# Kernel optimization log

Measured on AMD Instinct MI355X. Metric: run time of the kernel, lower is better.

## Reference

```python
import jax, jax.numpy as jnp
import numpy as np
from jax import lax

B, E, H, L, P, IMG, NCLS = 8, 768, 12, 12, 16, 224, 1000
D = E // H
MLP = 4 * E
SCALE = D ** -0.5
NPATCH = (IMG // P) ** 2  # 196
N = NPATCH + 1             # 197 with cls token
INIT_VAL = 0.1


def _ln(x, g, b, eps=1e-5):
    mu = jnp.mean(x, -1, keepdims=True)
    var = jnp.mean((x - mu) ** 2, -1, keepdims=True)
    return (x - mu) / jnp.sqrt(var + eps) * g + b


def _wasserstein(q, cov_q, k, cov_k):
    # 2-Wasserstein distance matrix between diagonal Gaussians (STOSA style)
    mean_term = (-2.0 * jnp.einsum('bhnd,bhmd->bhnm', q, k)
                 + jnp.sum(q * q, -1)[..., :, None]
                 + jnp.sum(k * k, -1)[..., None, :])
    sq_q = jnp.sqrt(jnp.clip(cov_q, 1e-24))
    sq_k = jnp.sqrt(jnp.clip(cov_k, 1e-24))
    cov_term = (-2.0 * jnp.einsum('bhnd,bhmd->bhnm', sq_q, sq_k)
                + jnp.sum(cov_q, -1)[..., :, None]
                + jnp.sum(cov_k, -1)[..., None, :])
    return mean_term + cov_term


def _patch_embed(x, w, b):
    # x: [B,3,IMG,IMG], w: [E,3,P,P] -> [B, NPATCH, E]
    y = lax.conv_general_dilated(x, w, (P, P), 'VALID',
                                 dimension_numbers=('NCHW', 'OIHW', 'NCHW'))
    y = y + b[None, :, None, None]
    return y.reshape(x.shape[0], E, -1).transpose(0, 2, 1)


def _mlp(x, w1, b1, w2, b2):
    return jax.nn.gelu(x @ w1.T + b1, approximate=False) @ w2.T + b2


def setup_inputs() -> dict:
    key = jax.random.key(0)
    ks = jax.random.split(key, 32)
    s = 0.02
    inp = {
        'x': jax.random.normal(ks[0], (B, 3, IMG, IMG), jnp.float32),
        'rel_pos_bias': jax.random.normal(ks[1], (H, N, N), jnp.float32),
        'patch_w': jax.random.normal(ks[2], (E, 3, P, P), jnp.float32) * s,
        'patch_b': jnp.zeros((E,), jnp.float32),
        'cov_patch_w': jax.random.normal(ks[3], (E, 3, P, P), jnp.float32) * s,
        'cov_patch_b': jnp.zeros((E,), jnp.float32),
        'cls_tok': jax.random.normal(ks[4], (1, 1, E), jnp.float32) * s,
        'cov_cls_tok': jax.random.normal(ks[5], (1, 1, E), jnp.float32) * s,
        'norm1_g': jnp.ones((L, E), jnp.float32),
        'norm1_b': jnp.zeros((L, E), jnp.float32),
        'qkv_w': jax.random.normal(ks[6], (L, 3 * E, E), jnp.float32) * s,
        'q_bias': jnp.zeros((L, E), jnp.float32),
        'v_bias': jnp.zeros((L, E), jnp.float32),
        'cov_q_bias': jnp.zeros((L, E), jnp.float32),
        'cov_v_bias': jnp.zeros((L, E), jnp.float32),
        'proj_w': jax.random.normal(ks[7], (L, E, E), jnp.float32) * s,
        'proj_b': jnp.zeros((L, E), jnp.float32),
        'cov_proj_w': jax.random.normal(ks[8], (L, E, E), jnp.float32) * s,
        'cov_proj_b': jnp.zeros((L, E), jnp.float32),
        'gamma1': jnp.full((L, E), INIT_VAL, jnp.float32),
        'gamma2': jnp.full((L, E), INIT_VAL, jnp.float32),
        'norm2_g': jnp.ones((L, E), jnp.float32),
        'norm2_b': jnp.zeros((L, E), jnp.float32),
        'fc1_w': jax.random.normal(ks[9], (L, MLP, E), jnp.float32) * s,
        'fc1_b': jnp.zeros((L, MLP), jnp.float32),
        'fc2_w': jax.random.normal(ks[10], (L, E, MLP), jnp.float32) * s,
        'fc2_b': jnp.zeros((L, E), jnp.float32),
        'fc_norm_g': jnp.ones((E,), jnp.float32),
        'fc_norm_b': jnp.zeros((E,), jnp.float32),
        'head_w': jax.random.normal(ks[11], (NCLS, E), jnp.float32) * s,
        'head_b': jnp.zeros((NCLS,), jnp.float32),
    }
    # fix_init_weight rescaling: proj / cov_proj / fc2 divided by sqrt(2*layer_id)
    resc = 1.0 / jnp.sqrt(2.0 * jnp.arange(1, L + 1, dtype=jnp.float32))
    inp['proj_w'] = inp['proj_w'] * resc[:, None, None]
    inp['cov_proj_w'] = inp['cov_proj_w'] * resc[:, None, None]
    inp['fc2_w'] = inp['fc2_w'] * resc[:, None, None]
    return inp


def reference(x, rel_pos_bias, patch_w, patch_b, cov_patch_w, cov_patch_b,
              cls_tok, cov_cls_tok, norm1_g, norm1_b, qkv_w, q_bias, v_bias,
              cov_q_bias, cov_v_bias, proj_w, proj_b, cov_proj_w, cov_proj_b,
              gamma1, gamma2, norm2_g, norm2_b, fc1_w, fc1_b, fc2_w, fc2_b,
              fc_norm_g, fc_norm_b, head_w, head_b):
    b = x.shape[0]
    xm = _patch_embed(x, patch_w, patch_b)
    xc = _patch_embed(x, cov_patch_w, cov_patch_b)
    xm = jnp.concatenate([jnp.broadcast_to(cls_tok, (b, 1, E)), xm], 1)
    xc = jnp.concatenate([jnp.broadcast_to(cov_cls_tok, (b, 1, E)), xc], 1)
    n = xm.shape[1]

    for i in range(L):
        xm_n = _ln(xm, norm1_g[i], norm1_b[i])
        xc_n = _ln(xc, norm1_g[i], norm1_b[i])  # shared norm1, as in source
        qkvb = jnp.concatenate([q_bias[i], jnp.zeros_like(v_bias[i]), v_bias[i]])
        cov_qkvb = jnp.concatenate([cov_q_bias[i], jnp.zeros_like(cov_v_bias[i]), cov_v_bias[i]])
        qkv = (xm_n @ qkv_w[i].T + qkvb).reshape(b, n, 3, H, D).transpose(2, 0, 3, 1, 4)
        q, k, v = qkv[0], qkv[1], qkv[2]
        # NOTE: source (bug-faithfully) uses qkv.weight for the cov path too
        cqkv = jax.nn.elu(xc_n @ qkv_w[i].T + cov_qkvb) + 1.0
        cqkv = cqkv.reshape(b, n, 3, H, D).transpose(2, 0, 3, 1, 4)
        cq, ck, cv = cqkv[0], cqkv[1], cqkv[2]
        q = q * SCALE
        attn = jax.nn.sigmoid(-_wasserstein(q, cq, k, ck) + 1e-24)
        attn = jax.nn.softmax(attn + rel_pos_bias, axis=-1)  # [B,H,N,N]
        mean_ctx = jnp.einsum('bhnm,bhmd->bhnd', attn, v).transpose(0, 2, 1, 3).reshape(b, n, E)
        cov_ctx = jnp.einsum('bhnm,bhmd->bhnd', attn * attn, cv).transpose(0, 2, 1, 3).reshape(b, n, E)
        mh = mean_ctx @ proj_w[i].T + proj_b[i]
        ch = cov_ctx @ cov_proj_w[i].T + cov_proj_b[i]
        xm = xm + gamma1[i] * mh
        xm = xm + gamma2[i] * _mlp(_ln(xm, norm2_g[i], norm2_b[i]), fc1_w[i], fc1_b[i], fc2_w[i], fc2_b[i])
        xc = xc + gamma1[i] * ch
        xc = xc + gamma2[i] * _mlp(_ln(xc, norm2_g[i], norm2_b[i]), fc1_w[i], fc1_b[i], fc2_w[i], fc2_b[i])

    t = jnp.mean(xm[:, 1:], axis=1)          # mean pooling over patch tokens
    t = _ln(t, fc_norm_g, fc_norm_b)
    return t @ head_w.T + head_b              # [B, num_classes]
```

## Files before the change

### kernel.cpp

```cpp
#include <hip/hip_runtime.h>
#include <hip/hip_bf16.h>
#include <math.h>

#define BB 8
#define EE 768
#define HH 12
#define LL 12
#define DD 64
#define MLPD 3072
#define NN 197
#define NPATCH 196
#define NCLS 1000
#define NROWS (BB*NN)
#define PROWS (BB*NPATCH)
#define MPAD 1664
#define HTILES 13
#define NBH (BB*HH)
#define NP224 224
#define NP256 256
#define SCALE 0.125f

#define MODE_F32   0
#define MODE_ELU1F 1
#define MODE_GELUB 2
#define MODE_RESF  3

typedef __attribute__((ext_vector_type(8))) short bf16x8;
typedef __attribute__((ext_vector_type(4))) float f32x4;

__device__ __forceinline__ unsigned short f2b(float f) {
    union { __hip_bfloat16 h; unsigned short u; } x;
    x.h = __float2bfloat16(f);
    return x.u;
}

#define GLD(gptr, lptr) __builtin_amdgcn_global_load_lds( \
    (const __attribute__((address_space(1))) unsigned int*)(gptr), \
    (__attribute__((address_space(3))) unsigned int*)(lptr), 16, 0, 0)

__global__ __launch_bounds__(256) void mfma_gemm2(
    const unsigned short* __restrict__ A0, const unsigned short* __restrict__ A1,
    const unsigned short* __restrict__ W0, const unsigned short* __restrict__ W1,
    const float* __restrict__ bias0, const float* __restrict__ bias1,
    int K, int Nc, int mode0, int mode1,
    const float* __restrict__ gamma,
    const float* __restrict__ resid0, const float* __restrict__ resid1,
    float* __restrict__ Cf0, float* __restrict__ Cf1,
    unsigned short* __restrict__ Cb0, unsigned short* __restrict__ Cb1)
{
    __shared__ unsigned short lA[128 * 32];
    __shared__ unsigned short lB[128 * 32];
    const int tid  = threadIdx.x;
    const int lane = tid & 63;
    const int wave = tid >> 6;
    const int wm = wave >> 1, wn = wave & 1;
    const int half = blockIdx.y >= HTILES;
    const int mout0 = (blockIdx.y - (half ? HTILES : 0)) * 128;
    const int n0 = blockIdx.x * 128;
    const unsigned short* A = half ? A1 : A0;
    const unsigned short* W = half ? W1 : W0;
    const float* bias = half ? bias1 : bias0;
    const float* resid = half ? resid1 : resid0;
    float* Cf = half ? Cf1 : Cf0;
    unsigned short* Cb = half ? Cb1 : Cb0;
    const int mode = half ? mode1 : mode0;

    const int srow  = lane >> 2;
    const int skoff = (lane & 3) * 8;
    const int fr = lane & 15;
    const int fk = (lane >> 4) * 8;

    f32x4 acc[4][4];
#pragma unroll
    for (int i = 0; i < 4; i++)
#pragma unroll
        for (int j = 0; j < 4; j++) acc[i][j] = (f32x4){0.f, 0.f, 0.f, 0.f};

    for (int k0 = 0; k0 < K; k0 += 32) {
#pragma unroll
        for (int i = 0; i < 2; i++) {
            int chunk = wave * 2 + i;
            int row = chunk * 16 + srow;
            GLD(A + (size_t)(mout0 + row) * K + k0 + skoff, lA + chunk * 512);
            GLD(W + (size_t)(n0 + row) * K + k0 + skoff, lB + chunk * 512);
        }
        __syncthreads();
        bf16x8 a[4], b[4];
#pragma unroll
        for (int t = 0; t < 4; t++) {
            a[t] = *(const bf16x8*)(lA + (wm * 64 + t * 16 + fr) * 32 + fk);
            b[t] = *(const bf16x8*)(lB + (wn * 64 + t * 16 + fr) * 32 + fk);
        }
#pragma unroll
        for (int i = 0; i < 4; i++)
#pragma unroll
            for (int j = 0; j < 4; j++)
                acc[i][j] = __builtin_amdgcn_mfma_f32_16x16x32_bf16(a[i], b[j], acc[i][j], 0, 0, 0);
        __syncthreads();
    }

    const int crow0 = mout0 + wm * 64;
    const int ccol0 = n0 + wn * 64;
    const int lr = (lane >> 4) * 4;
    const int lc = lane & 15;
#pragma unroll
    for (int i = 0; i < 4; i++) {
#pragma unroll
        for (int j = 0; j < 4; j++) {
            int col = ccol0 + j * 16 + lc;
            float bv = bias ? bias[col] : 0.f;
#pragma unroll
            for (int r = 0; r < 4; r++) {
                int row = crow0 + i * 16 + lr + r;
                float v = acc[i][j][r] + bv;
                size_t o = (size_t)row * Nc + col;
                if (mode == MODE_ELU1F) {
                    Cf[o] = (v > 0.f) ? (v + 1.f) : expf(v);
                } else if (mode == MODE_GELUB) {
                    v = 0.5f * v * (1.f + erff(v * 0.70710678118654752f));
                    Cb[o] = f2b(v);
                } else if (mode == MODE_RESF) {
                    Cf[o] = resid[o] + gamma[col] * v;
                } else {
                    Cf[o] = v;
                }
            }
        }
    }
}

__global__ __launch_bounds__(256) void mfma_gemm2_sk(
    const unsigned short* __restrict__ A0, const unsigned short* __restrict__ A1,
    const unsigned short* __restrict__ W0, const unsigned short* __restrict__ W1,
    int K, int Kc, int Nc, int S,
    float* __restrict__ P)
{
    __shared__ unsigned short lA[128 * 32];
    __shared__ unsigned short lB[128 * 32];
    const int tid  = threadIdx.x;
    const int lane = tid & 63;
    const int wave = tid >> 6;
    const int wm = wave >> 1, wn = wave & 1;
    const int half = blockIdx.y >= HTILES;
    const int mout0 = (blockIdx.y - (half ? HTILES : 0)) * 128;
    const int n0 = blockIdx.x * 128;
    const int z = blockIdx.z;
    const int kb = z * Kc;
    const unsigned short* A = half ? A1 : A0;
    const unsigned short* W = half ? W1 : W0;

    const int srow  = lane >> 2;
    const int skoff = (lane & 3) * 8;
    const int fr = lane & 15;
    const int fk = (lane >> 4) * 8;

    f32x4 acc[4][4];
#pragma unroll
    for (int i = 0; i < 4; i++)
#pragma unroll
        for (int j = 0; j < 4; j++) acc[i][j] = (f32x4){0.f, 0.f, 0.f, 0.f};

    for (int k0 = kb; k0 < kb + Kc; k0 += 32) {
#pragma unroll
        for (int i = 0; i < 2; i++) {
            int chunk = wave * 2 + i;
            int row = chunk * 16 + srow;
            GLD(A + (size_t)(mout0 + row) * K + k0 + skoff, lA + chunk * 512);
            GLD(W + (size_t)(n0 + row) * K + k0 + skoff, lB + chunk * 512);
        }
        __syncthreads();
        bf16x8 a[4], b[4];
#pragma unroll
        for (int t = 0; t < 4; t++) {
            a[t] = *(const bf16x8*)(lA + (wm * 64 + t * 16 + fr) * 32 + fk);
            b[t] = *(const bf16x8*)(lB + (wn * 64 + t * 16 + fr) * 32 + fk);
        }
#pragma unroll
        for (int i = 0; i < 4; i++)
#pragma unroll
            for (int j = 0; j < 4; j++)
                acc[i][j] = __builtin_amdgcn_mfma_f32_16x16x32_bf16(a[i], b[j], acc[i][j], 0, 0, 0);
        __syncthreads();
    }

    float* Pout = P + (size_t)(half * S + z) * MPAD * Nc;
    const int crow0 = mout0 + wm * 64;
    const int ccol0 = n0 + wn * 64;
    const int lr = (lane >> 4) * 4;
    const int lc = lane & 15;
#pragma unroll
    for (int i = 0; i < 4; i++) {
#pragma unroll
        for (int j = 0; j < 4; j++) {
            int col = ccol0 + j * 16 + lc;
#pragma unroll
            for (int r = 0; r < 4; r++) {
                int row = crow0 + i * 16 + lr + r;
                Pout[(size_t)row * Nc + col] = acc[i][j][r];
            }
        }
    }
}

__global__ __launch_bounds__(256) void sk_reduce_kernel(
    const float* __restrict__ P, int S, int Nc, int mode,
    const float* __restrict__ bias0, const float* __restrict__ bias1,
    const float* __restrict__ gamma,
    const float* __restrict__ resid0, const float* __restrict__ resid1,
    float* __restrict__ C0, float* __restrict__ C1)
{
    const size_t per = (size_t)MPAD * Nc;
    size_t gi = ((size_t)blockIdx.x * 256 + threadIdx.x) * 4;
    if (gi >= per) return;
    const int half = blockIdx.y;
    const float* p = P + (size_t)half * S * per + gi;
    float4 s = *(const float4*)p;
    for (int z = 1; z < S; z++) {
        float4 q = *(const float4*)(p + (size_t)z * per);
        s.x += q.x; s.y += q.y; s.z += q.z; s.w += q.w;
    }
    const int col = (int)(gi % (size_t)Nc);
    const float* bias = half ? bias1 : bias0;
    float4 bv = *(const float4*)(bias + col);
    s.x += bv.x; s.y += bv.y; s.z += bv.z; s.w += bv.w;
    float* C = half ? C1 : C0;
    if (mode == MODE_RESF) {
        const float* resid = half ? resid1 : resid0;
        float4 rv = *(const float4*)(resid + gi);
        float4 gv = *(const float4*)(gamma + col);
        s.x = rv.x + gv.x * s.x;
        s.y = rv.y + gv.y * s.y;
        s.z = rv.z + gv.z * s.z;
        s.w = rv.w + gv.w * s.w;
    }
    *(float4*)(C + gi) = s;
}

__global__ __launch_bounds__(256) void pre_kernel(
    const float* __restrict__ qkv, const float* __restrict__ cqkv,
    unsigned short* __restrict__ Aq, unsigned short* __restrict__ Bk,
    float* __restrict__ rsum, float* __restrict__ csum,
    unsigned short* __restrict__ vT, unsigned short* __restrict__ cvT)
{
    const int t = blockIdx.x;
    const int bh = blockIdx.y;
    const int b = bh / HH, h = bh % HH;
    const int n0 = t * 64;
    const int lane = threadIdx.x & 63;
    const int w = threadIdx.x >> 6;
    __shared__ unsigned short vs[64][66];
    __shared__ unsigned short cvs[64][66];

    for (int p = 0; p < 16; p++) {
        int nl = p * 4 + w;
        int n = n0 + nl;
        int d = lane;
        size_t arow = ((size_t)bh * NP256 + n) * 128;
        if (n < NN) {
            size_t basei = (size_t)(b * NN + n) * 3 * EE + h * DD + d;
            float q  = qkv[basei];
            float k  = qkv[basei + EE];
            float v  = qkv[basei + 2 * EE];
            float cq = cqkv[basei];
            float ck = cqkv[basei + EE];
            float cv = cqkv[basei + 2 * EE];
            float qs = q * SCALE;
            float sqq = sqrtf(fmaxf(cq, 1e-24f));
            float sqk = sqrtf(fmaxf(ck, 1e-24f));
            Aq[arow + d]      = f2b(qs);
            Aq[arow + 64 + d] = f2b(sqq);
            Bk[arow + d]      = f2b(k);
            Bk[arow + 64 + d] = f2b(sqk);
            vs[nl][d]  = f2b(v);
            cvs[nl][d] = f2b(cv);
            float r = qs * qs + cq;
            float c = k * k + ck;
            for (int off2 = 32; off2 > 0; off2 >>= 1) {
                r += __shfl_down(r, off2);
                c += __shfl_down(c, off2);
            }
            if (d == 0) { rsum[bh * NP256 + n] = r; csum[bh * NP256 + n] = c; }
        } else {
            ((unsigned int*)(Aq + arow))[d] = 0u;
            ((unsigned int*)(Bk + arow))[d] = 0u;
            vs[nl][d] = 0; cvs[nl][d] = 0;
            if (d == 0) { rsum[bh * NP256 + n] = 0.f; csum[bh * NP256 + n] = 0.f; }
        }
    }
    __syncthreads();
    for (int p = 0; p < 16; p++) {
        int dr = p * 4 + w;
        int n = n0 + lane;
        if (n < NP224) {
            vT [((size_t)bh * 64 + dr) * NP224 + n] = vs[lane][dr];
            cvT[((size_t)bh * 64 + dr) * NP224 + n] = cvs[lane][dr];
        }
    }
}

__global__ __launch_bounds__(256) void wass_gemm(
    const unsigned short* __restrict__ Aq, const unsigned short* __restrict__ Bk,
    const float* __restrict__ rsum, const float* __restrict__ csum,
    const float* __restrict__ rpb, float* __restrict__ S)
{
    __shared__ unsigned short lA[128 * 32];
    __shared__ unsigned short lB[128 * 32];
    const int tid = threadIdx.x, lane = tid & 63, wave = tid >> 6;
    const int wm = wave >> 1, wn = wave & 1;
    const int bh = blockIdx.z;
    const int h = bh % HH;
    const int m0 = blockIdx.y * 128;
    const int n0 = blockIdx.x * 128;
    const unsigned short* A = Aq + (size_t)bh * NP256 * 128;
    const unsigned short* B = Bk + (size_t)bh * NP256 * 128;
    const int srow = lane >> 2, skoff = (lane & 3) * 8;
    const int fr = lane & 15, fk = (lane >> 4) * 8;

    f32x4 acc[4][4];
#pragma unroll
    for (int i = 0; i < 4; i++)
#pragma unroll
        for (int j = 0; j < 4; j++) acc[i][j] = (f32x4){0.f, 0.f, 0.f, 0.f};

    for (int k0 = 0; k0 < 128; k0 += 32) {
#pragma unroll
        for (int i = 0; i < 2; i++) {
            int chunk = wave * 2 + i;
            int row = chunk * 16 + srow;
            GLD(A + (size_t)(m0 + row) * 128 + k0 + skoff, lA + chunk * 512);
            GLD(B + (size_t)(n0 + row) * 128 + k0 + skoff, lB + chunk * 512);
        }
        __syncthreads();
        bf16x8 a[4], b[4];
#pragma unroll
        for (int t = 0; t < 4; t++) {
            a[t] = *(const bf16x8*)(lA + (wm * 64 + t * 16 + fr) * 32 + fk);
            b[t] = *(const bf16x8*)(lB + (wn * 64 + t * 16 + fr) * 32 + fk);
        }
#pragma unroll
        for (int i = 0; i < 4; i++)
#pragma unroll
            for (int j = 0; j < 4; j++)
                acc[i][j] = __builtin_amdgcn_mfma_f32_16x16x32_bf16(a[i], b[j], acc[i][j], 0, 0, 0);
        __syncthreads();
    }

    const int lr = (lane >> 4) * 4;
    const int lc = lane & 15;
#pragma unroll
    for (int i = 0; i < 4; i++) {
#pragma unroll
        for (int j = 0; j < 4; j++) {
            int m = n0 + wn * 64 + j * 16 + lc;
            float cs = csum[bh * NP256 + m];
#pragma unroll
            for (int r = 0; r < 4; r++) {
                int n = m0 + wm * 64 + i * 16 + lr + r;
                float z = 2.f * acc[i][j][r] - rsum[bh * NP256 + n] - cs + 1e-24f;
                float s = 1.f / (1.f + expf(-z));
                float rp = (n < NN && m < NN) ? rpb[((size_t)h * NN + n) * NN + m] : 0.f;
                S[((size_t)bh * NP256 + n) * NP256 + m] = s + rp;
            }
        }
    }
}

__global__ __launch_bounds__(256) void softmax_kernel(
    const float* __restrict__ S, unsigned short* __restrict__ Ab,
    unsigned short* __restrict__ A2b)
{
    const int wave = threadIdx.x >> 6, lane = threadIdx.x & 63;
    const int idx = blockIdx.x * 4 + wave;
    if (idx >= NBH * NN) return;
    const int bh = idx / NN, n = idx % NN;
    const float* row = S + ((size_t)bh * NP256 + n) * NP256;
    float l[4], mx = -1e30f;
#pragma unroll
    for (int j = 0; j < 4; j++) {
        int m = lane + j * 64;
        l[j] = (m < NN) ? row[m] : -1e30f;
        mx = fmaxf(mx, l[j]);
    }
    for (int off = 32; off > 0; off >>= 1) mx = fmaxf(mx, __shfl_xor(mx, off));
    float e[4], sum = 0.f;
#pragma unroll
    for (int j = 0; j < 4; j++) {
        int m = lane + j * 64;
        e[j] = (m < NN) ? expf(l[j] - mx) : 0.f;
        sum += e[j];
    }
    for (int off = 32; off > 0; off >>= 1) sum += __shfl_xor(sum, off);
    float inv = 1.f / sum;
    unsigned short* ar  = Ab  + ((size_t)bh * NP256 + n) * NP224;
    unsigned short* ar2 = A2b + ((size_t)bh * NP256 + n) * NP224;
#pragma unroll
    for (int j = 0; j < 4; j++) {
        int m = lane + j * 64;
        if (m < NP224) {
            float p = e[j] * inv;
            ar[m]  = f2b(p);
            ar2[m] = f2b(p * p);
        }
    }
}

__global__ __launch_bounds__(256) void ctx_gemm(
    const unsigned short* __restrict__ Ab, const unsigned short* __restrict__ A2b,
    const unsigned short* __restrict__ vT, const unsigned short* __restrict__ cvT,
    unsigned short* __restrict__ ctxm, unsigned short* __restrict__ ctxc)
{
    __shared__ unsigned short lA1[128 * 32];
    __shared__ unsigned short lA2[128 * 32];
    __shared__ unsigned short lB[128 * 32];
    const int tid = threadIdx.x, lane = tid & 63, wave = tid >> 6;
    const int wm = wave >> 1, wn = wave & 1;
    const int bh = blockIdx.y;
    const int b = bh / HH, h = bh % HH;
    const int m0 = blockIdx.x * 128;
    const int srow = lane >> 2, skoff = (lane & 3) * 8;
    const int fr = lane & 15, fk = (lane >> 4) * 8;

    f32x4 acc[4][4];
#pragma unroll
    for (int i = 0; i < 4; i++)
#pragma unroll
        for (int j = 0; j < 4; j++) acc[i][j] = (f32x4){0.f, 0.f, 0.f, 0.f};

    for (int k0 = 0; k0 < NP224; k0 += 32) {
#pragma unroll
        for (int i = 0; i < 2; i++) {
            int chunk = wave * 2 + i;
            int row = chunk * 16 + srow;
            size_t aoff = ((size_t)bh * NP256 + m0 + row) * NP224 + k0 + skoff;
            GLD(Ab + aoff,  lA1 + chunk * 512);
            GLD(A2b + aoff, lA2 + chunk * 512);
            const unsigned short* bsrc = (chunk < 4)
                ? (vT  + ((size_t)bh * 64 + row) * NP224)
                : (cvT + ((size_t)bh * 64 + row - 64) * NP224);
            GLD(bsrc + k0 + skoff, lB + chunk * 512);
        }
        __syncthreads();
        const unsigned short* asrc = wn ? lA2 : lA1;
        bf16x8 a[4], bfr[4];
#pragma unroll
        for (int t = 0; t < 4; t++) {
            a[t]   = *(const bf16x8*)(asrc + (wm * 64 + t * 16 + fr) * 32 + fk);
            bfr[t] = *(const bf16x8*)(lB   + (wn * 64 + t * 16 + fr) * 32 + fk);
        }
#pragma unroll
        for (int i = 0; i < 4; i++)
#pragma unroll
            for (int j = 0; j < 4; j++)
                acc[i][j] = __builtin_amdgcn_mfma_f32_16x16x32_bf16(a[i], bfr[j], acc[i][j], 0, 0, 0);
        __syncthreads();
    }

    const int lr = (lane >> 4) * 4;
    const int lc = lane & 15;
    unsigned short* dst = wn ? ctxc : ctxm;
#pragma unroll
    for (int i = 0; i < 4; i++) {
#pragma unroll
        for (int j = 0; j < 4; j++) {
            int dcol = j * 16 + lc;
#pragma unroll
            for (int r = 0; r < 4; r++) {
                int n = m0 + wm * 64 + i * 16 + lr + r;
                if (n >= NN) continue;
                dst[((size_t)(b * NN + n)) * EE + h * DD + dcol] = f2b(acc[i][j][r]);
            }
        }
    }
}

__global__ __launch_bounds__(256) void gemm_kernel(
    const float* __restrict__ A, const float* __restrict__ W,
    const float* __restrict__ bias, float* __restrict__ C,
    int M, int Nc, int K)
{
    __shared__ float As[16][64];
    __shared__ float Bs[16][64];
    const int tid = threadIdx.x;
    const int tm = tid >> 4;
    const int tn = tid & 15;
    const int m0 = blockIdx.y * 64;
    const int n0 = blockIdx.x * 64;
    float acc[4][4] = {};
    for (int k0 = 0; k0 < K; k0 += 16) {
#pragma unroll
        for (int i = 0; i < 4; i++) {
            int idx = tid + i * 256;
            int r = idx >> 4;
            int c = idx & 15;
            int gm = m0 + r;
            As[c][r] = (gm < M) ? A[(size_t)gm * K + k0 + c] : 0.f;
            int gn = n0 + r;
            Bs[c][r] = (gn < Nc) ? W[(size_t)gn * K + k0 + c] : 0.f;
        }
        __syncthreads();
#pragma unroll
        for (int kk = 0; kk < 16; kk++) {
            float a[4], b[4];
#pragma unroll
            for (int i = 0; i < 4; i++) a[i] = As[kk][tm * 4 + i];
#pragma unroll
            for (int j = 0; j < 4; j++) b[j] = Bs[kk][tn * 4 + j];
#pragma unroll
            for (int i = 0; i < 4; i++)
#pragma unroll
                for (int j = 0; j < 4; j++)
                    acc[i][j] += a[i] * b[j];
        }
        __syncthreads();
    }
#pragma unroll
    for (int i = 0; i < 4; i++) {
        int gm = m0 + tm * 4 + i;
        if (gm >= M) continue;
#pragma unroll
        for (int j = 0; j < 4; j++) {
            int gn = n0 + tn * 4 + j;
            if (gn >= Nc) continue;
            C[(size_t)gm * Nc + gn] = acc[i][j] + (bias ? bias[gn] : 0.f);
        }
    }
}

__global__ __launch_bounds__(256) void cvt_kernel(
    const float* __restrict__ src, unsigned short* __restrict__ dst, int n)
{
    int i = (blockIdx.x * 256 + threadIdx.x) * 4;
    if (i >= n) return;
    float4 f = *(const float4*)(src + i);
    ushort4 u;
    u.x = f2b(f.x); u.y = f2b(f.y); u.z = f2b(f.z); u.w = f2b(f.w);
    *(ushort4*)(dst + i) = u;
}

#define W_QKV   0
#define W_PROJ  1769472
#define W_CPROJ 2359296
#define W_FC1   2949120
#define W_FC2   5308416
#define W_TOTAL 7667712

__global__ __launch_bounds__(256) void cvt_layer_kernel(
    const float* __restrict__ qkvw, const float* __restrict__ pw,
    const float* __restrict__ cpw, const float* __restrict__ f1,
    const float* __restrict__ f2, unsigned short* __restrict__ dst)
{
    int i = (blockIdx.x * 256 + threadIdx.x) * 4;
    if (i >= W_TOTAL) return;
    const float* s; int off;
    if (i < W_PROJ)        { s = qkvw; off = W_QKV; }
    else if (i < W_CPROJ)  { s = pw;   off = W_PROJ; }
    else if (i < W_FC1)    { s = cpw;  off = W_CPROJ; }
    else if (i < W_FC2)    { s = f1;   off = W_FC1; }
    else                   { s = f2;   off = W_FC2; }
    float4 f = *(const float4*)(s + (i - off));
    ushort4 u;
    u.x = f2b(f.x); u.y = f2b(f.y); u.z = f2b(f.z); u.w = f2b(f.w);
    *(ushort4*)(dst + i) = u;
}

__global__ __launch_bounds__(256) void im2col_kernel(
    const float* __restrict__ x, unsigned short* __restrict__ col)
{
    int idx = blockIdx.x * 256 + threadIdx.x;
    if (idx >= PROWS * EE) return;
    int c = idx % EE;
    int r = idx / EE;
    int b = r / NPATCH;
    int p = r % NPATCH;
    int ph = p / 14, pw = p % 14;
    int ch = c >> 8;
    int rem = c & 255;
    int i = rem >> 4, j = rem & 15;
    col[idx] = f2b(x[(((size_t)b * 3 + ch) * 224 + (ph * 16 + i)) * 224 + (pw * 16 + j)]);
}

__global__ __launch_bounds__(256) void assemble_kernel(
    const float* __restrict__ tm, const float* __restrict__ tc,
    const float* __restrict__ cls, const float* __restrict__ ccls,
    float* __restrict__ xm, float* __restrict__ xc)
{
    int idx = blockIdx.x * 256 + threadIdx.x;
    if (idx >= NROWS * EE) return;
    int e = idx % EE;
    int r = idx / EE;
    int b = r / NN, n = r % NN;
    if (n == 0) {
        xm[idx] = cls[e];
        xc[idx] = ccls[e];
    } else {
        size_t s = ((size_t)(b * NPATCH + n - 1)) * EE + e;
        xm[idx] = tm[s];
        xc[idx] = tc[s];
    }
}

__global__ __launch_bounds__(256) void ln2_kernel(
    const float* __restrict__ xm, const float* __restrict__ xc,
    unsigned short* __restrict__ y, const float* __restrict__ g,
    const float* __restrict__ bb)
{
    int row = blockIdx.x;
    int tid = threadIdx.x;
    const float* src;
    size_t orow;
    if (row < NROWS) { src = xm + (size_t)row * EE; orow = row; }
    else { src = xc + (size_t)(row - NROWS) * EE; orow = (size_t)(row - NROWS) + MPAD; }
    __shared__ float red[256];
    float v0 = src[tid], v1 = src[tid + 256], v2 = src[tid + 512];
    red[tid] = v0 + v1 + v2;
    __syncthreads();
    for (int s = 128; s > 0; s >>= 1) { if (tid < s) red[tid] += red[tid + s]; __syncthreads(); }
    float mu = red[0] * (1.f / 768.f);
    __syncthreads();
    float d0 = v0 - mu, d1 = v1 - mu, d2 = v2 - mu;
    red[tid] = d0 * d0 + d1 * d1 + d2 * d2;
    __syncthreads();
    for (int s = 128; s > 0; s >>= 1) { if (tid < s) red[tid] += red[tid + s]; __syncthreads(); }
    float rstd = rsqrtf(red[0] * (1.f / 768.f) + 1e-5f);
    unsigned short* yr = y + orow * EE;
    yr[tid]       = f2b(d0 * rstd * g[tid]       + bb[tid]);
    yr[tid + 256] = f2b(d1 * rstd * g[tid + 256] + bb[tid + 256]);
    yr[tid + 512] = f2b(d2 * rstd * g[tid + 512] + bb[tid + 512]);
}

__global__ __launch_bounds__(256) void qkvbias_kernel(
    const float* __restrict__ qb, const float* __restrict__ vb,
    const float* __restrict__ cqb, const float* __restrict__ cvb,
    float* __restrict__ bm, float* __restrict__ bc)
{
    int j = blockIdx.x * 256 + threadIdx.x;
    if (j >= 3 * EE) return;
    float m, c;
    if (j < EE)        { m = qb[j];        c = cqb[j]; }
    else if (j < 2*EE) { m = 0.f;          c = 0.f; }
    else               { m = vb[j - 2*EE]; c = cvb[j - 2*EE]; }
    bm[j] = m;
    bc[j] = c;
}

__global__ __launch_bounds__(256) void pool_ln_kernel(
    const float* __restrict__ xm, float* __restrict__ out,
    const float* __restrict__ g, const float* __restrict__ bb)
{
    int b = blockIdx.x;
    int tid = threadIdx.x;
    __shared__ float red[256];
    float p[3];
#pragma unroll
    for (int i = 0; i < 3; i++) {
        int e = tid + i * 256;
        float s = 0.f;
        for (int n = 1; n < NN; n++) s += xm[((size_t)(b * NN + n)) * EE + e];
        p[i] = s * (1.f / 196.f);
    }
    red[tid] = p[0] + p[1] + p[2];
    __syncthreads();
    for (int s = 128; s > 0; s >>= 1) { if (tid < s) red[tid] += red[tid + s]; __syncthreads(); }
    float mu = red[0] * (1.f / 768.f);
    __syncthreads();
    float d0 = p[0] - mu, d1 = p[1] - mu, d2 = p[2] - mu;
    red[tid] = d0 * d0 + d1 * d1 + d2 * d2;
    __syncthreads();
    for (int s = 128; s > 0; s >>= 1) { if (tid < s) red[tid] += red[tid + s]; __syncthreads(); }
    float rstd = rsqrtf(red[0] * (1.f / 768.f) + 1e-5f);
    out[(size_t)b * EE + tid]       = d0 * rstd * g[tid]       + bb[tid];
    out[(size_t)b * EE + tid + 256] = d1 * rstd * g[tid + 256] + bb[tid + 256];
    out[(size_t)b * EE + tid + 512] = d2 * rstd * g[tid + 512] + bb[tid + 512];
}

extern "C" void kernel_launch(void* const* d_in, const int* in_sizes, int n_in,
                              void* d_out, int out_size, void* d_ws, size_t ws_size,
                              hipStream_t stream)
{
    const float* x        = (const float*)d_in[0];
    const float* rpb      = (const float*)d_in[1];
    const float* patch_w  = (const float*)d_in[2];
    const float* patch_b  = (const float*)d_in[3];
    const float* cpatch_w = (const float*)d_in[4];
    const float* cpatch_b = (const float*)d_in[5];
    const float* cls_tok  = (const float*)d_in[6];
    const float* ccls_tok = (const float*)d_in[7];
    const float* norm1_g  = (const float*)d_in[8];
    const float* norm1_b  = (const float*)d_in[9];
    const float* qkv_w    = (const float*)d_in[10];
    const float* q_bias   = (const float*)d_in[11];
    const float* v_bias   = (const float*)d_in[12];
    const float* cq_bias  = (const float*)d_in[13];
    const float* cv_bias  = (const float*)d_in[14];
    const float* proj_w   = (const float*)d_in[15];
    const float* proj_b   = (const float*)d_in[16];
    const float* cproj_w  = (const float*)d_in[17];
    const float* cproj_b  = (const float*)d_in[18];
    const float* gamma1   = (const float*)d_in[19];
    const float* gamma2   = (const float*)d_in[20];
    const float* norm2_g  = (const float*)d_in[21];
    const float* norm2_b  = (const float*)d_in[22];
    const float* fc1_w    = (const float*)d_in[23];
    const float* fc1_b    = (const float*)d_in[24];
    const float* fc2_w    = (const float*)d_in[25];
    const float* fc2_b    = (const float*)d_in[26];
    const float* fcn_g    = (const float*)d_in[27];
    const float* fcn_b    = (const float*)d_in[28];
    const float* head_w   = (const float*)d_in[29];
    const float* head_b   = (const float*)d_in[30];
    float* out = (float*)d_out;

    char* base = (char*)d_ws;
    size_t off = 0;
    auto alloc = [&](size_t bytes) {
        void* p = base + off;
        off = (off + bytes + 255) & ~(size_t)255;
        return p;
    };
    unsigned short* wbuf  = (unsigned short*)alloc((size_t)W_TOTAL * 2);
    unsigned short* pw_m  = (unsigned short*)alloc((size_t)589824 * 2);
    unsigned short* pw_c  = (unsigned short*)alloc((size_t)589824 * 2);
    float* xm   = (float*)alloc((size_t)MPAD * EE * 4);
    float* xc   = (float*)alloc((size_t)MPAD * EE * 4);
    unsigned short* xn2 = (unsigned short*)alloc((size_t)2 * MPAD * EE * 2);
    float* qkv  = (float*)alloc((size_t)MPAD * 3 * EE * 4);
    float* cqkv = (float*)alloc((size_t)MPAD * 3 * EE * 4);
    char*  un   = (char*)alloc((size_t)NBH * NP256 * NP256 * 4);
    float* S    = (float*)un;
    unsigned short* hbuf = (unsigned short*)un;
    unsigned short* Aq  = (unsigned short*)alloc((size_t)NBH * NP256 * 128 * 2);
    unsigned short* Bk  = (unsigned short*)alloc((size_t)NBH * NP256 * 128 * 2);
    unsigned short* vT  = (unsigned short*)alloc((size_t)NBH * 64 * NP224 * 2);
    unsigned short* cvT = (unsigned short*)alloc((size_t)NBH * 64 * NP224 * 2);
    float* rsum = (float*)alloc((size_t)NBH * NP256 * 4);
    float* csum = (float*)alloc((size_t)NBH * NP256 * 4);
    unsigned short* ctx2 = (unsigned short*)alloc((size_t)2 * MPAD * EE * 2);
    unsigned short* colb = (unsigned short*)alloc((size_t)MPAD * EE * 2);
    float* biasq  = (float*)alloc(3 * EE * 4);
    float* biasc  = (float*)alloc(3 * EE * 4);
    float* pooled = (float*)alloc((size_t)BB * EE * 4);
    float* pbuf = (float*)alloc((size_t)2 * 4 * MPAD * EE * 4);
    unsigned short* Ab  = (unsigned short*)qkv;
    unsigned short* A2b = (unsigned short*)cqkv;
    float* tm = qkv;
    float* tc = cqkv;
    unsigned short* ctxm = ctx2;
    unsigned short* ctxc = ctx2 + (size_t)MPAD * EE;

    dim3 t256(256);
    dim3 gridRed(MPAD * EE / 1024, 2);

    cvt_kernel<<<dim3(589824 / 4 / 256), t256, 0, stream>>>(patch_w, pw_m, 589824);
    cvt_kernel<<<dim3(589824 / 4 / 256), t256, 0, stream>>>(cpatch_w, pw_c, 589824);
    im2col_kernel<<<dim3((PROWS * EE + 255) / 256), t256, 0, stream>>>(x, colb);
    mfma_gemm2_sk<<<dim3(EE / 128, 2 * HTILES, 3), t256, 0, stream>>>(
        colb, colb, pw_m, pw_c, EE, 256, EE, 3, pbuf);
    sk_reduce_kernel<<<gridRed, t256, 0, stream>>>(
        pbuf, 3, EE, MODE_F32, patch_b, cpatch_b, nullptr, nullptr, nullptr, tm, tc);
    assemble_kernel<<<dim3((NROWS * EE + 255) / 256), t256, 0, stream>>>(
        tm, tc, cls_tok, ccls_tok, xm, xc);

    dim3 gridQKV(3 * EE / 128, 2 * HTILES);
    dim3 gridMLP(MLPD / 128, 2 * HTILES);
    dim3 gridPre(4, NBH);
    dim3 gridWass(2, 2, NBH);
    dim3 gridSm((NBH * NN + 3) / 4);
    dim3 gridCtx(2, NBH);
    dim3 gridCvtL((W_TOTAL / 4 + 255) / 256);
    dim3 gridLN(2 * NROWS);
    const unsigned short* xn2c = xn2 + (size_t)MPAD * EE;
    const unsigned short* hbufc = hbuf + (size_t)MPAD * MLPD;

    for (int l = 0; l < LL; l++) {
        cvt_layer_kernel<<<gridCvtL, t256, 0, stream>>>(
            qkv_w + (size_t)l * 3 * EE * EE, proj_w + (size_t)l * EE * EE,
            cproj_w + (size_t)l * EE * EE, fc1_w + (size_t)l * MLPD * EE,
            fc2_w + (size_t)l * EE * MLPD, wbuf);
        qkvbias_kernel<<<dim3(9), t256, 0, stream>>>(
            q_bias + l * EE, v_bias + l * EE, cq_bias + l * EE, cv_bias + l * EE,
            biasq, biasc);

        ln2_kernel<<<gridLN, t256, 0, stream>>>(xm, xc, xn2, norm1_g + l * EE, norm1_b + l * EE);
        mfma_gemm2<<<gridQKV, t256, 0, stream>>>(
            xn2, xn2c, wbuf + W_QKV, wbuf + W_QKV, biasq, biasc, EE, 3 * EE,
            MODE_F32, MODE_ELU1F, nullptr, nullptr, nullptr, qkv, cqkv, nullptr, nullptr);

        pre_kernel<<<gridPre, t256, 0, stream>>>(qkv, cqkv, Aq, Bk, rsum, csum, vT, cvT);
        wass_gemm<<<gridWass, t256, 0, stream>>>(Aq, Bk, rsum, csum, rpb, S);
        softmax_kernel<<<gridSm, t256, 0, stream>>>(S, Ab, A2b);
        ctx_gemm<<<gridCtx, t256, 0, stream>>>(Ab, A2b, vT, cvT, ctxm, ctxc);

        mfma_gemm2_sk<<<dim3(EE / 128, 2 * HTILES, 3), t256, 0, stream>>>(
            ctxm, ctxc, wbuf + W_PROJ, wbuf + W_CPROJ, EE, 256, EE, 3, pbuf);
        sk_reduce_kernel<<<gridRed, t256, 0, stream>>>(
            pbuf, 3, EE, MODE_RESF, proj_b + l * EE, cproj_b + l * EE,
            gamma1 + l * EE, xm, xc, xm, xc);

        ln2_kernel<<<gridLN, t256, 0, stream>>>(xm, xc, xn2, norm2_g + l * EE, norm2_b + l * EE);
        mfma_gemm2<<<gridMLP, t256, 0, stream>>>(
            xn2, xn2c, wbuf + W_FC1, wbuf + W_FC1, fc1_b + l * MLPD, fc1_b + l * MLPD,
            EE, MLPD, MODE_GELUB, MODE_GELUB, nullptr, nullptr, nullptr,
            nullptr, nullptr, hbuf, hbuf + (size_t)MPAD * MLPD);
        mfma_gemm2_sk<<<dim3(EE / 128, 2 * HTILES, 4), t256, 0, stream>>>(
            hbuf, hbufc, wbuf + W_FC2, wbuf + W_FC2, MLPD, 768, EE, 4, pbuf);
        sk_reduce_kernel<<<gridRed, t256, 0, stream>>>(
            pbuf, 4, EE, MODE_RESF, fc2_b + l * EE, fc2_b + l * EE,
            gamma2 + l * EE, xm, xc, xm, xc);
    }

    pool_ln_kernel<<<dim3(BB), t256, 0, stream>>>(xm, pooled, fcn_g, fcn_b);
    {
        dim3 grid((NCLS + 63) / 64, (BB + 63) / 64);
        gemm_kernel<<<grid, t256, 0, stream>>>(pooled, head_w, head_b, out, BB, NCLS, EE);
    }
}
```

Measured before the change: 3.222 ms.

## Fuse Wasserstein scores, softmax and context GEMMs into one attention kernel

Replaces the three-kernel attention path (score GEMM writing fp32 S, row softmax, context GEMM) with one kernel per 64-query tile. It computes scores with MFMA, does the sigmoid, bias and softmax in registers, keeps the probabilities in LDS as bf16, and squares them on the fly for the covariance path. This removes the large fp32 score buffer round trip and two launches per layer, at the cost of fewer blocks (4x96) and extra LDS per block. The classifier head GEMM is also replaced with a simple wave-per-output dot-product kernel.

```diff
diff --git a/kernel.cpp b/kernel.cpp
--- a/kernel.cpp
+++ b/kernel.cpp
@@ -32,6 +32,12 @@
     union { __hip_bfloat16 h; unsigned short u; } x;
     x.h = __float2bfloat16(f);
     return x.u;
+}
+
+__device__ __forceinline__ float b2f(unsigned short u) {
+    union { unsigned int i; float f; } x;
+    x.i = ((unsigned int)u) << 16;
+    return x.f;
 }
 
 #define GLD(gptr, lptr) __builtin_amdgcn_global_load_lds( \
@@ -298,232 +304,151 @@
     }
 }
 
-__global__ __launch_bounds__(256) void wass_gemm(
+#define PADW 232
+__global__ __launch_bounds__(256) void attn_fused(
     const unsigned short* __restrict__ Aq, const unsigned short* __restrict__ Bk,
     const float* __restrict__ rsum, const float* __restrict__ csum,
-    const float* __restrict__ rpb, float* __restrict__ S)
-{
-    __shared__ unsigned short lA[128 * 32];
-    __shared__ unsigned short lB[128 * 32];
-    const int tid = threadIdx.x, lane = tid & 63, wave = tid >> 6;
-    const int wm = wave >> 1, wn = wave & 1;
-    const int bh = blockIdx.z;
-    const int h = bh % HH;
-    const int m0 = blockIdx.y * 128;
-    const int n0 = blockIdx.x * 128;
+    const float* __restrict__ rpb,
+    const unsigned short* __restrict__ vT, const unsigned short* __restrict__ cvT,
+    unsigned short* __restrict__ ctxm, unsigned short* __restrict__ ctxc)
+{
+    __shared__ unsigned short lA[64 * 32];
+    __shared__ unsigned short lB[256 * 32];
+    __shared__ unsigned short lB2[128 * 32];
+    __shared__ unsigned short pL[64 * PADW];
+    const int tid = threadIdx.x, lane = tid & 63, w = tid >> 6;
+    const int bh = blockIdx.y;
+    const int b = bh / HH, h = bh % HH;
+    const int q0 = blockIdx.x * 64;
+    const int srow = lane >> 2, skoff = (lane & 3) * 8;
+    const int fr = lane & 15, fk = (lane >> 4) * 8;
+    const int lr4 = (lane >> 4) * 4;
     const unsigned short* A = Aq + (size_t)bh * NP256 * 128;
     const unsigned short* B = Bk + (size_t)bh * NP256 * 128;
-    const int srow = lane >> 2, skoff = (lane & 3) * 8;
-    const int fr = lane & 15, fk = (lane >> 4) * 8;
-
-    f32x4 acc[4][4];
-#pragma unroll
-    for (int i = 0; i < 4; i++)
-#pragma unroll
-        for (int j = 0; j < 4; j++) acc[i][j] = (f32x4){0.f, 0.f, 0.f, 0.f};
+
+    f32x4 accS[16];
+#pragma unroll
+    for (int j = 0; j < 16; j++) accS[j] = (f32x4){0.f, 0.f, 0.f, 0.f};
 
     for (int k0 = 0; k0 < 128; k0 += 32) {
+        GLD(A + (size_t)(q0 + w * 16 + srow) * 128 + k0 + skoff, lA + w * 512);
+#pragma unroll
+        for (int i = 0; i < 4; i++) {
+            int chunk = w * 4 + i;
+            GLD(B + (size_t)(chunk * 16 + srow) * 128 + k0 + skoff, lB + chunk * 512);
+        }
+        __syncthreads();
+        bf16x8 a = *(const bf16x8*)(lA + (w * 16 + fr) * 32 + fk);
+#pragma unroll
+        for (int j = 0; j < 16; j++) {
+            bf16x8 bb = *(const bf16x8*)(lB + (j * 16 + fr) * 32 + fk);
+            accS[j] = __builtin_amdgcn_mfma_f32_16x16x32_bf16(a, bb, accS[j], 0, 0, 0);
+        }
+        __syncthreads();
+    }
+
+    float rs[4];
+#pragma unroll
+    for (int r = 0; r < 4; r++) rs[r] = rsum[bh * NP256 + q0 + w * 16 + lr4 + r];
+    float cs[16];
+#pragma unroll
+    for (int j = 0; j < 16; j++) cs[j] = csum[bh * NP256 + j * 16 + fr];
+
+#pragma unroll
+    for (int r = 0; r < 4; r++) {
+        int rowg = q0 + w * 16 + lr4 + r;
+        float v[16];
+#pragma unroll
+        for (int j = 0; j < 16; j++) {
+            int col = j * 16 + fr;
+            float z = 2.f * accS[j][r] - rs[r] - cs[j] + 1e-24f;
+            float s = 1.f / (1.f + expf(-z));
+            float rp = (col < NN && rowg < NN) ? rpb[((size_t)h * NN + rowg) * NN + col] : 0.f;
+            v[j] = (col < NN) ? (s + rp) : -1e30f;
+        }
+        float mx = -1e30f;
+#pragma unroll
+        for (int j = 0; j < 16; j++) mx = fmaxf(mx, v[j]);
+        mx = fmaxf(mx, __shfl_xor(mx, 1));
+        mx = fmaxf(mx, __shfl_xor(mx, 2));
+        mx = fmaxf(mx, __shfl_xor(mx, 4));
+        mx = fmaxf(mx, __shfl_xor(mx, 8));
+        float sum = 0.f;
+#pragma unroll
+        for (int j = 0; j < 16; j++) { v[j] = expf(v[j] - mx); sum += v[j]; }
+        sum += __shfl_xor(sum, 1);
+        sum += __shfl_xor(sum, 2);
+        sum += __shfl_xor(sum, 4);
+        sum += __shfl_xor(sum, 8);
+        float inv = 1.f / sum;
+        int rowl = w * 16 + lr4 + r;
+#pragma unroll
+        for (int j = 0; j < 14; j++)
+            pL[rowl * PADW + j * 16 + fr] = f2b(v[j] * inv);
+    }
+
+    f32x4 acc2[2][4];
+#pragma unroll
+    for (int p = 0; p < 2; p++)
+#pragma unroll
+        for (int j = 0; j < 4; j++) acc2[p][j] = (f32x4){0.f, 0.f, 0.f, 0.f};
+
+    for (int k0 = 0; k0 < NP224; k0 += 32) {
 #pragma unroll
         for (int i = 0; i < 2; i++) {
-            int chunk = wave * 2 + i;
-            int row = chunk * 16 + srow;
-            GLD(A + (size_t)(m0 + row) * 128 + k0 + skoff, lA + chunk * 512);
-            GLD(B + (size_t)(n0 + row) * 128 + k0 + skoff, lB + chunk * 512);
+            int chunk = w * 2 + i;
+            const unsigned short* src = (chunk < 4)
+                ? (vT  + ((size_t)bh * 64 + chunk * 16 + srow) * NP224)
+                : (cvT + ((size_t)bh * 64 + (chunk - 4) * 16 + srow) * NP224);
+            GLD(src + k0 + skoff, lB2 + chunk * 512);
         }
         __syncthreads();
-        bf16x8 a[4], b[4];
-#pragma unroll
-        for (int t = 0; t < 4; t++) {
-            a[t] = *(const bf16x8*)(lA + (wm * 64 + t * 16 + fr) * 32 + fk);
-            b[t] = *(const bf16x8*)(lB + (wn * 64 + t * 16 + fr) * 32 + fk);
-        }
-#pragma unroll
-        for (int i = 0; i < 4; i++)
-#pragma unroll
-            for (int j = 0; j < 4; j++)
-                acc[i][j] = __builtin_amdgcn_mfma_f32_16x16x32_bf16(a[i], b[j], acc[i][j], 0, 0, 0);
+        bf16x8 ap = *(const bf16x8*)(pL + (w * 16 + fr) * PADW + k0 + fk);
+        bf16x8 ap2;
+#pragma unroll
+        for (int e = 0; e < 8; e++) {
+            float pv = b2f((unsigned short)ap[e]);
+            ap2[e] = (short)f2b(pv * pv);
+        }
+#pragma unroll
+        for (int j = 0; j < 4; j++) {
+            bf16x8 bv = *(const bf16x8*)(lB2 + (j * 16 + fr) * 32 + fk);
+            bf16x8 bc = *(const bf16x8*)(lB2 + ((64 + j * 16) + fr) * 32 + fk);
+            acc2[0][j] = __builtin_amdgcn_mfma_f32_16x16x32_bf16(ap,  bv, acc2[0][j], 0, 0, 0);
+            acc2[1][j] = __builtin_amdgcn_mfma_f32_16x16x32_bf16(ap2, bc, acc2[1][j], 0, 0, 0);
+        }
         __syncthreads();
     }
 
-    const int lr = (lane >> 4) * 4;
-    const int lc = lane & 15;
-#pragma unroll
-    for (int i = 0; i < 4; i++) {
-#pragma unroll
-        for (int j = 0; j < 4; j++) {
-            int m = n0 + wn * 64 + j * 16 + lc;
-            float cs = csum[bh * NP256 + m];
-#pragma unroll
-            for (int r = 0; r < 4; r++) {
-                int n = m0 + wm * 64 + i * 16 + lr + r;
-                float z = 2.f * acc[i][j][r] - rsum[bh * NP256 + n] - cs + 1e-24f;
-                float s = 1.f / (1.f + expf(-z));
-                float rp = (n < NN && m < NN) ? rpb[((size_t)h * NN + n) * NN + m] : 0.f;
-                S[((size_t)bh * NP256 + n) * NP256 + m] = s + rp;
-            }
-        }
-    }
-}
-
-__global__ __launch_bounds__(256) void softmax_kernel(
-    const float* __restrict__ S, unsigned short* __restrict__ Ab,
-    unsigned short* __restrict__ A2b)
-{
-    const int wave = threadIdx.x >> 6, lane = threadIdx.x & 63;
-    const int idx = blockIdx.x * 4 + wave;
-    if (idx >= NBH * NN) return;
-    const int bh = idx / NN, n = idx % NN;
-    const float* row = S + ((size_t)bh * NP256 + n) * NP256;
-    float l[4], mx = -1e30f;
 #pragma unroll
     for (int j = 0; j < 4; j++) {
-        int m = lane + j * 64;
-        l[j] = (m < NN) ? row[m] : -1e30f;
-        mx = fmaxf(mx, l[j]);
-    }
-    for (int off = 32; off > 0; off >>= 1) mx = fmaxf(mx, __shfl_xor(mx, off));
-    float e[4], sum = 0.f;
-#pragma unroll
-    for (int j = 0; j < 4; j++) {
-        int m = lane + j * 64;
-        e[j] = (m < NN) ? expf(l[j] - mx) : 0.f;
-        sum += e[j];
-    }
-    for (int off = 32; off > 0; off >>= 1) sum += __shfl_xor(sum, off);
-    float inv = 1.f / sum;
-    unsigned short* ar  = Ab  + ((size_t)bh * NP256 + n) * NP224;
-    unsigned short* ar2 = A2b + ((size_t)bh * NP256 + n) * NP224;
-#pragma unroll
-    for (int j = 0; j < 4; j++) {
-        int m = lane + j * 64;
-        if (m < NP224) {
-            float p = e[j] * inv;
-            ar[m]  = f2b(p);
-            ar2[m] = f2b(p * p);
-        }
-    }
-}
-
-__global__ __launch_bounds__(256) void ctx_gemm(
-    const unsigned short* __restrict__ Ab, const unsigned short* __restrict__ A2b,
-    const unsigned short* __restrict__ vT, const unsigned short* __restrict__ cvT,
-    unsigned short* __restrict__ ctxm, unsigned short* __restrict__ ctxc)
-{
-    __shared__ unsigned short lA1[128 * 32];
-    __shared__ unsigned short lA2[128 * 32];
-    __shared__ unsigned short lB[128 * 32];
-    const int tid = threadIdx.x, lane = tid & 63, wave = tid >> 6;
-    const int wm = wave >> 1, wn = wave & 1;
-    const int bh = blockIdx.y;
-    const int b = bh / HH, h = bh % HH;
-    const int m0 = blockIdx.x * 128;
-    const int srow = lane >> 2, skoff = (lane & 3) * 8;
-    const int fr = lane & 15, fk = (lane >> 4) * 8;
-
-    f32x4 acc[4][4];
-#pragma unroll
-    for (int i = 0; i < 4; i++)
-#pragma unroll
-        for (int j = 0; j < 4; j++) acc[i][j] = (f32x4){0.f, 0.f, 0.f, 0.f};
-
-    for (int k0 = 0; k0 < NP224; k0 += 32) {
-#pragma unroll
-        for (int i = 0; i < 2; i++) {
-            int chunk = wave * 2 + i;
-            int row = chunk * 16 + srow;
-            size_t aoff = ((size_t)bh * NP256 + m0 + row) * NP224 + k0 + skoff;
-            GLD(Ab + aoff,  lA1 + chunk * 512);
-            GLD(A2b + aoff, lA2 + chunk * 512);
-            const unsigned short* bsrc = (chunk < 4)
-                ? (vT  + ((size_t)bh * 64 + row) * NP224)
-                : (cvT + ((size_t)bh * 64 + row - 64) * NP224);
-            GLD(bsrc + k0 + skoff, lB + chunk * 512);
-        }
-        __syncthreads();
-        const unsigned short* asrc = wn ? lA2 : lA1;
-        bf16x8 a[4], bfr[4];
-#pragma unroll
-        for (int t = 0; t < 4; t++) {
-            a[t]   = *(const bf16x8*)(asrc + (wm * 64 + t * 16 + fr) * 32 + fk);
-            bfr[t] = *(const bf16x8*)(lB   + (wn * 64 + t * 16 + fr) * 32 + fk);
-        }
-#pragma unroll
-        for (int i = 0; i < 4; i++)
-#pragma unroll
-            for (int j = 0; j < 4; j++)
-                acc[i][j] = __builtin_amdgcn_mfma_f32_16x16x32_bf16(a[i], bfr[j], acc[i][j], 0, 0, 0);
-        __syncthreads();
-    }
-
-    const int lr = (lane >> 4) * 4;
-    const int lc = lane & 15;
-    unsigned short* dst = wn ? ctxc : ctxm;
-#pragma unroll
-    for (int i = 0; i < 4; i++) {
-#pragma unroll
-        for (int j = 0; j < 4; j++) {
-            int dcol = j * 16 + lc;
-#pragma unroll
-            for (int r = 0; r < 4; r++) {
-                int n = m0 + wm * 64 + i * 16 + lr + r;
-                if (n >= NN) continue;
-                dst[((size_t)(b * NN + n)) * EE + h * DD + dcol] = f2b(acc[i][j][r]);
-            }
-        }
-    }
-}
-
-__global__ __launch_bounds__(256) void gemm_kernel(
-    const float* __restrict__ A, const float* __restrict__ W,
-    const float* __restrict__ bias, float* __restrict__ C,
-    int M, int Nc, int K)
-{
-    __shared__ float As[16][64];
-    __shared__ float Bs[16][64];
-    const int tid = threadIdx.x;
-    const int tm = tid >> 4;
-    const int tn = tid & 15;
-    const int m0 = blockIdx.y * 64;
-    const int n0 = blockIdx.x * 64;
-    float acc[4][4] = {};
-    for (int k0 = 0; k0 < K; k0 += 16) {
-#pragma unroll
-        for (int i = 0; i < 4; i++) {
-            int idx = tid + i * 256;
-            int r = idx >> 4;
-            int c = idx & 15;
-            int gm = m0 + r;
-            As[c][r] = (gm < M) ? A[(size_t)gm * K + k0 + c] : 0.f;
-            int gn = n0 + r;
-            Bs[c][r] = (gn < Nc) ? W[(size_t)gn * K + k0 + c] : 0.f;
-        }
-        __syncthreads();
-#pragma unroll
-        for (int kk = 0; kk < 16; kk++) {
-            float a[4], b[4];
-#pragma unroll
-            for (int i = 0; i < 4; i++) a[i] = As[kk][tm * 4 + i];
-#pragma unroll
-            for (int j = 0; j < 4; j++) b[j] = Bs[kk][tn * 4 + j];
-#pragma unroll
-            for (int i = 0; i < 4; i++)
-#pragma unroll
-                for (int j = 0; j < 4; j++)
-                    acc[i][j] += a[i] * b[j];
-        }
-        __syncthreads();
-    }
-#pragma unroll
-    for (int i = 0; i < 4; i++) {
-        int gm = m0 + tm * 4 + i;
-        if (gm >= M) continue;
-#pragma unroll
-        for (int j = 0; j < 4; j++) {
-            int gn = n0 + tn * 4 + j;
-            if (gn >= Nc) continue;
-            C[(size_t)gm * Nc + gn] = acc[i][j] + (bias ? bias[gn] : 0.f);
-        }
-    }
+        int d = j * 16 + fr;
+#pragma unroll
+        for (int r = 0; r < 4; r++) {
+            int n = q0 + w * 16 + lr4 + r;
+            if (n >= NN) continue;
+            size_t o = ((size_t)(b * NN + n)) * EE + h * DD + d;
+            ctxm[o] = f2b(acc2[0][j][r]);
+            ctxc[o] = f2b(acc2[1][j][r]);
+        }
+    }
+}
+
+__global__ __launch_bounds__(256) void head_kernel(
+    const float* __restrict__ pooled, const float* __restrict__ W,
+    const float* __restrict__ bias, float* __restrict__ out)
+{
+    const int wv = threadIdx.x >> 6, lane = threadIdx.x & 63;
+    const int c = blockIdx.x * 4 + wv;
+    const int b = blockIdx.y;
+    if (c >= NCLS) return;
+    const float* wr = W + (size_t)c * EE;
+    const float* pr = pooled + (size_t)b * EE;
+    float s = 0.f;
+#pragma unroll
+    for (int i = 0; i < 12; i++) s += pr[lane + i * 64] * wr[lane + i * 64];
+    for (int off = 32; off > 0; off >>= 1) s += __shfl_down(s, off);
+    if (lane == 0) out[(size_t)b * NCLS + c] = s + bias[c];
 }
 
 __global__ __launch_bounds__(256) void cvt_kernel(
@@ -725,9 +650,7 @@
     unsigned short* xn2 = (unsigned short*)alloc((size_t)2 * MPAD * EE * 2);
     float* qkv  = (float*)alloc((size_t)MPAD * 3 * EE * 4);
     float* cqkv = (float*)alloc((size_t)MPAD * 3 * EE * 4);
-    char*  un   = (char*)alloc((size_t)NBH * NP256 * NP256 * 4);
-    float* S    = (float*)un;
-    unsigned short* hbuf = (unsigned short*)un;
+    unsigned short* hbuf = (unsigned short*)alloc((size_t)2 * MPAD * MLPD * 2);
     unsigned short* Aq  = (unsigned short*)alloc((size_t)NBH * NP256 * 128 * 2);
     unsigned short* Bk  = (unsigned short*)alloc((size_t)NBH * NP256 * 128 * 2);
     unsigned short* vT  = (unsigned short*)alloc((size_t)NBH * 64 * NP224 * 2);
@@ -740,8 +663,6 @@
     float* biasc  = (float*)alloc(3 * EE * 4);
     float* pooled = (float*)alloc((size_t)BB * EE * 4);
     float* pbuf = (float*)alloc((size_t)2 * 4 * MPAD * EE * 4);
-    unsigned short* Ab  = (unsigned short*)qkv;
-    unsigned short* A2b = (unsigned short*)cqkv;
     float* tm = qkv;
     float* tc = cqkv;
     unsigned short* ctxm = ctx2;
@@ -763,9 +684,7 @@
     dim3 gridQKV(3 * EE / 128, 2 * HTILES);
     dim3 gridMLP(MLPD / 128, 2 * HTILES);
     dim3 gridPre(4, NBH);
-    dim3 gridWass(2, 2, NBH);
-    dim3 gridSm((NBH * NN + 3) / 4);
-    dim3 gridCtx(2, NBH);
+    dim3 gridAttn(4, NBH);
     dim3 gridCvtL((W_TOTAL / 4 + 255) / 256);
     dim3 gridLN(2 * NROWS);
     const unsigned short* xn2c = xn2 + (size_t)MPAD * EE;
@@ -786,9 +705,7 @@
             MODE_F32, MODE_ELU1F, nullptr, nullptr, nullptr, qkv, cqkv, nullptr, nullptr);
 
         pre_kernel<<<gridPre, t256, 0, stream>>>(qkv, cqkv, Aq, Bk, rsum, csum, vT, cvT);
-        wass_gemm<<<gridWass, t256, 0, stream>>>(Aq, Bk, rsum, csum, rpb, S);
-        softmax_kernel<<<gridSm, t256, 0, stream>>>(S, Ab, A2b);
-        ctx_gemm<<<gridCtx, t256, 0, stream>>>(Ab, A2b, vT, cvT, ctxm, ctxc);
+        attn_fused<<<gridAttn, t256, 0, stream>>>(Aq, Bk, rsum, csum, rpb, vT, cvT, ctxm, ctxc);
 
         mfma_gemm2_sk<<<dim3(EE / 128, 2 * HTILES, 3), t256, 0, stream>>>(
             ctxm, ctxc, wbuf + W_PROJ, wbuf + W_CPROJ, EE, 256, EE, 3, pbuf);
@@ -809,8 +726,5 @@
     }
 
     pool_ln_kernel<<<dim3(BB), t256, 0, stream>>>(xm, pooled, fcn_g, fcn_b);
-    {
-        dim3 grid((NCLS + 63) / 64, (BB + 63) / 64);
-        gemm_kernel<<<grid, t256, 0, stream>>>(pooled, head_w, head_b, out, BB, NCLS, EE);
-    }
-}
+    head_kernel<<<dim3((NCLS + 3) / 4, BB), t256, 0, stream>>>(pooled, head_w, head_b, out);
+}
```

Measured after the change: 2.880 ms. -10.6%, faster.
